# Performance work log

Measured on AMD Instinct MI355X. Metric: run time of the kernel, lower is better.

Reference implementation:

```python
import jax, jax.numpy as jnp
import numpy as np

B, T, D, VQ, L2, HID = 8, 2048, 768, 64, 12, 1024
K = 2 ** L2          # 4096 codebook entries
N_MID = 4            # condition_layer=6 -> 1 input + 4 middle + 1 output Linear, 5 BatchNorms
EPS_N = 1e-6
EPS_BN = 1e-5


def setup_inputs() -> dict:
    key = jax.random.key(0)
    ks = jax.random.split(key, 10)
    g = lambda i, shape, sc: jax.random.normal(ks[i], shape, jnp.float32) * sc
    return {
        "h_in": jax.random.normal(ks[0], (B, D, T), jnp.float32),
        "attn_mask": jax.random.randint(ks[1], (B, T), 0, 2, jnp.int32),
        "proj_w": g(2, (VQ, D), 0.02), "proj_b": jnp.zeros((VQ,), jnp.float32),
        "inv_w": g(3, (D, VQ), 0.02), "inv_b": jnp.zeros((D,), jnp.float32),
        "mlp_w_in": g(4, (HID, L2), 0.1), "mlp_b_in": jnp.zeros((HID,), jnp.float32),
        "mlp_w_mid": g(5, (N_MID, HID, HID), 0.03), "mlp_b_mid": jnp.zeros((N_MID, HID), jnp.float32),
        "mlp_w_out": g(6, (VQ, HID), 0.03), "mlp_b_out": jnp.zeros((VQ,), jnp.float32),
        "bn_gamma": jnp.ones((N_MID + 1, HID), jnp.float32),
        "bn_beta": jnp.zeros((N_MID + 1, HID), jnp.float32),
    }


def _bn(x, gamma, beta):
    # BatchNorm1d, training mode: batch mean / biased var over codebook rows
    m = x.mean(axis=0)
    v = x.var(axis=0)
    return (x - m) * jax.lax.rsqrt(v + EPS_BN) * gamma + beta


def _l2norm(x):
    return x / (jnp.linalg.norm(x, axis=-1, keepdims=True) + EPS_N)


def reference(h_in, attn_mask, proj_w, proj_b, inv_w, inv_b,
              mlp_w_in, mlp_b_in, mlp_w_mid, mlp_b_mid, mlp_w_out, mlp_b_out,
              bn_gamma, bn_beta):
    # --- codebook: binary vectors -> condition MLP (Linear+BN+ReLU x5, Linear) ---
    ints = jnp.arange(K)
    bits = ((ints[:, None] & (1 << jnp.arange(L2 - 1, -1, -1))) > 0).astype(jnp.float32)  # [K, L2]
    x = jax.nn.relu(_bn(bits @ mlp_w_in.T + mlp_b_in, bn_gamma[0], bn_beta[0]))
    for i in range(N_MID):
        x = jax.nn.relu(_bn(x @ mlp_w_mid[i].T + mlp_b_mid[i], bn_gamma[i + 1], bn_beta[i + 1]))
    embed = x @ mlp_w_out.T + mlp_b_out          # [K, VQ]
    embed = _l2norm(embed)                        # sphere=True

    # --- project hidden states: h_in [B,D,T] -> [B,T,VQ] ---
    h = jnp.einsum('bdt,vd->btv', h_in, proj_w) + proj_b
    h = _l2norm(h)

    # --- pairwise squared distances to codebook, argmax of -d (== softmax argmax) ---
    hf = h.reshape(-1, VQ)                                       # [B*T, VQ]
    d = (hf ** 2).sum(-1, keepdims=True) + (embed ** 2).sum(-1) - 2.0 * (hf @ embed.T)  # [B*T, K]
    code = jnp.argmax(-d, axis=-1)                               # [B*T]

    # --- masked gather/scatter quantization (eval path: hard codes) ---
    mask = (attn_mask == 1)                                      # [B, T]
    h_vq = embed[code].reshape(B, T, VQ) * mask[..., None].astype(h.dtype)
    quantized = jnp.einsum('btv,dv->btd', h_vq, inv_w) + inv_b   # proj_inv -> [B, T, D]
    vq_code = jnp.where(mask, code.reshape(B, T), 0)
    return quantized, vq_code
```

## Files before the change

kernel.cpp:

```cpp
#include <hip/hip_runtime.h>
#include <stddef.h>

#define BB   8
#define TT_  2048
#define DD   768
#define VQ_  64
#define L2C  12
#define HID_ 1024
#define KK   4096
#define NMID 4
#define NT   (BB*TT_)

typedef _Float16 h8v __attribute__((ext_vector_type(8)));
typedef float    f4v __attribute__((ext_vector_type(4)));

#define GL16(g, l) __builtin_amdgcn_global_load_lds( \
    (const __attribute__((address_space(1))) void*)(g), \
    (__attribute__((address_space(3))) void*)(l), 16, 0, 0)

__global__ __launch_bounds__(256) void k_mlp_in(const float* __restrict__ w_in,
                                                const float* __restrict__ b_in,
                                                float* __restrict__ X) {
    __shared__ float ws_[256 * 12];
    __shared__ float bs_[256];
    int tid = threadIdx.x;
    int h0  = blockIdx.x * 256;
    for (int i = tid; i < 256 * 12; i += 256) ws_[i] = w_in[h0 * 12 + i];
    bs_[tid] = b_in[h0 + tid];
    __syncthreads();
    float w[12];
#pragma unroll
    for (int l = 0; l < 12; l++) w[l] = ws_[tid * 12 + l];
    float bias = bs_[tid];
    int k0 = blockIdx.y * 16;
    for (int kk = 0; kk < 16; kk++) {
        int k = k0 + kk;
        float acc = bias;
#pragma unroll
        for (int l = 0; l < 12; l++)
            if ((k >> (11 - l)) & 1) acc += w[l];
        X[(size_t)k * HID_ + h0 + tid] = acc;
    }
}

__global__ __launch_bounds__(256) void k_bn_stats1(const float* __restrict__ Y,
                                                   float* __restrict__ part) {
    int b = blockIdx.x;
    int c = blockIdx.y * 256 + threadIdx.x;
    const float* src = Y + ((size_t)b << 6) * HID_ + c;
    float s = 0.f, q = 0.f;
    for (int r = 0; r < 64; r++) {
        float v = src[(size_t)r << 10];
        s += v; q += v * v;
    }
    part[((size_t)b << 10) + c] = s;
    part[65536 + ((size_t)b << 10) + c] = q;
}

__global__ __launch_bounds__(256) void k_bn_stats2(const float* __restrict__ part,
                                                   float* __restrict__ mv) {
    int c = blockIdx.x * 256 + threadIdx.x;
    float s = 0.f, q = 0.f;
    for (int b = 0; b < 64; b++) {
        s += part[((size_t)b << 10) + c];
        q += part[65536 + ((size_t)b << 10) + c];
    }
    float m = s * (1.f / KK);
    float v = q * (1.f / KK) - m * m;
    mv[c] = m; mv[HID_ + c] = v;
}

__global__ __launch_bounds__(256) void k_bn_apply_split(const float* __restrict__ Y,
                                                        const float* __restrict__ mv,
                                                        const float* __restrict__ gamma,
                                                        const float* __restrict__ beta,
                                                        _Float16* __restrict__ Xhi,
                                                        _Float16* __restrict__ Xlo) {
    int i = blockIdx.x * 256 + threadIdx.x;
    int c = (i << 2) & (HID_ - 1);
    float4 x = ((const float4*)Y)[i];
    float4 m = *(const float4*)(mv + c);
    float4 v = *(const float4*)(mv + HID_ + c);
    float4 g = *(const float4*)(gamma + c);
    float4 b = *(const float4*)(beta + c);
    float o[4];
    o[0] = fmaxf(0.f, (x.x - m.x) * (1.f / sqrtf(v.x + 1e-5f)) * g.x + b.x);
    o[1] = fmaxf(0.f, (x.y - m.y) * (1.f / sqrtf(v.y + 1e-5f)) * g.y + b.y);
    o[2] = fmaxf(0.f, (x.z - m.z) * (1.f / sqrtf(v.z + 1e-5f)) * g.z + b.z);
    o[3] = fmaxf(0.f, (x.w - m.w) * (1.f / sqrtf(v.w + 1e-5f)) * g.w + b.w);
    union { _Float16 h[4]; uint2 u; } uh, ul;
#pragma unroll
    for (int j = 0; j < 4; j++) {
        _Float16 h = (_Float16)o[j];
        uh.h[j] = h;
        ul.h[j] = (_Float16)(o[j] - (float)h);
    }
    *(uint2*)(Xhi + ((size_t)i << 2)) = uh.u;
    *(uint2*)(Xlo + ((size_t)i << 2)) = ul.u;
}

__global__ __launch_bounds__(256) void k_gemm_mfma2(const _Float16* __restrict__ Ahi,
                                                    const _Float16* __restrict__ Alo,
                                                    const _Float16* __restrict__ Whi,
                                                    const _Float16* __restrict__ Wlo,
                                                    const float* __restrict__ bias,
                                                    float* __restrict__ C,
                                                    int M, int N, int Kd) {
    __shared__ __attribute__((aligned(128))) char lds[2][24576];
    const int tid = threadIdx.x;
    int wg = blockIdx.x;
    const int nwg = gridDim.x;
    wg = (wg & 7) * (nwg >> 3) + (wg >> 3);
    const int nx = M >> 7;
    const int m0 = (wg % nx) << 7;
    const int n0 = (wg / nx) << 6;
    const int wave = tid >> 6, lane = tid & 63;
    const int l15 = lane & 15, quad = lane >> 4;
    const int wm = (wave >> 1) << 6;
    const int wn = (wave & 1) << 5;

    const int pA0 = ((wave << 1) | 0) * 1024 + lane * 16;
    const int pA1 = ((wave << 1) | 1) * 1024 + lane * 16;
    const int pW  = wave * 1024 + lane * 16;
    const int qA0 = pA0 ^ (((pA0 >> 7) & 3) << 4);
    const int qA1 = pA1 ^ (((pA1 >> 7) & 3) << 4);
    const int qW  = pW  ^ (((pW  >> 7) & 3) << 4);
    const size_t krow = (size_t)Kd * 2;
    const char* gAh0 = (const char*)Ahi + (size_t)(m0 + (qA0 >> 6)) * krow + (qA0 & 63);
    const char* gAh1 = (const char*)Ahi + (size_t)(m0 + (qA1 >> 6)) * krow + (qA1 & 63);
    const char* gAl0 = (const char*)Alo + (size_t)(m0 + (qA0 >> 6)) * krow + (qA0 & 63);
    const char* gAl1 = (const char*)Alo + (size_t)(m0 + (qA1 >> 6)) * krow + (qA1 & 63);
    const char* gWh  = (const char*)Whi + (size_t)(n0 + (qW >> 6)) * krow + (qW & 63);
    const char* gWl  = (const char*)Wlo + (size_t)(n0 + (qW >> 6)) * krow + (qW & 63);
    const int dA0 = (wave << 1) * 1024;
    const int dA1 = dA0 + 1024;
    const int dW  = wave * 1024;

    int offA[4], offW[2];
#pragma unroll
    for (int i = 0; i < 4; i++) {
        int r = wm + (i << 4) + l15;
        offA[i] = r * 64 + ((quad ^ ((r >> 1) & 3)) << 4);
    }
#pragma unroll
    for (int j = 0; j < 2; j++) {
        int r = wn + (j << 4) + l15;
        offW[j] = r * 64 + ((quad ^ ((r >> 1) & 3)) << 4);
    }

    f4v acc[4][2];
#pragma unroll
    for (int i = 0; i < 4; i++)
#pragma unroll
        for (int j = 0; j < 2; j++) acc[i][j] = (f4v){0.f, 0.f, 0.f, 0.f};

#define STAGE(bufi, tt) do { \
        char* b_ = lds[bufi]; size_t o_ = (size_t)(tt) << 6; \
        GL16(gAh0 + o_, b_ + dA0); \
        GL16(gAh1 + o_, b_ + dA1); \
        GL16(gAl0 + o_, b_ + 8192 + dA0); \
        GL16(gAl1 + o_, b_ + 8192 + dA1); \
        GL16(gWh  + o_, b_ + 16384 + dW); \
        GL16(gWl  + o_, b_ + 20480 + dW); \
    } while (0)

    STAGE(0, 0);
    const int nt = Kd >> 5;
    for (int t = 0; t < nt; ++t) {
        const int cur = t & 1;
        if (t + 1 < nt) {
            STAGE(cur ^ 1, t + 1);
            asm volatile("s_waitcnt vmcnt(6)" ::: "memory");
        } else {
            asm volatile("s_waitcnt vmcnt(0)" ::: "memory");
        }
        __builtin_amdgcn_s_barrier();
        asm volatile("" ::: "memory");
        const char* b = lds[cur];
        h8v ah[4], al[4], bh[2], bl[2];
#pragma unroll
        for (int i = 0; i < 4; i++) {
            ah[i] = *(const h8v*)(b + offA[i]);
            al[i] = *(const h8v*)(b + 8192 + offA[i]);
        }
#pragma unroll
        for (int j = 0; j < 2; j++) {
            bh[j] = *(const h8v*)(b + 16384 + offW[j]);
            bl[j] = *(const h8v*)(b + 20480 + offW[j]);
        }
        __builtin_amdgcn_s_setprio(1);
#pragma unroll
        for (int i = 0; i < 4; i++)
#pragma unroll
            for (int j = 0; j < 2; j++) {
                acc[i][j] = __builtin_amdgcn_mfma_f32_16x16x32_f16(ah[i], bh[j], acc[i][j], 0, 0, 0);
                acc[i][j] = __builtin_amdgcn_mfma_f32_16x16x32_f16(ah[i], bl[j], acc[i][j], 0, 0, 0);
                acc[i][j] = __builtin_amdgcn_mfma_f32_16x16x32_f16(al[i], bh[j], acc[i][j], 0, 0, 0);
            }
        __builtin_amdgcn_s_setprio(0);
        asm volatile("" ::: "memory");
        __builtin_amdgcn_s_barrier();
    }
#undef STAGE

#pragma unroll
    for (int j = 0; j < 2; j++) {
        int col = n0 + wn + (j << 4) + l15;
        float bv = bias[col];
#pragma unroll
        for (int i = 0; i < 4; i++) {
            int row = m0 + wm + (i << 4) + (quad << 2);
#pragma unroll
            for (int r = 0; r < 4; r++)
                C[(size_t)(row + r) * N + col] = acc[i][j][r] + bv;
        }
    }
}

__global__ __launch_bounds__(256) void k_l2norm(float* __restrict__ E,
                                                float* __restrict__ eqh,
                                                _Float16* __restrict__ Ehi,
                                                _Float16* __restrict__ Elo) {
    int tid = threadIdx.x;
    int row = blockIdx.x * 4 + (tid >> 6);
    int v = tid & 63;
    size_t off = ((size_t)row << 6) + v;
    float x = E[off];
    float ss = x * x;
#pragma unroll
    for (int o = 32; o; o >>= 1) ss += __shfl_xor(ss, o, 64);
    float inv = 1.f / (sqrtf(ss) + 1e-6f);
    float xn = x * inv;
    E[off] = xn;
    _Float16 hh = (_Float16)xn;
    Ehi[off] = hh;
    Elo[off] = (_Float16)(xn - (float)hh);
    if (v == 0) eqh[row] = -0.5f * (ss * inv * inv);
}

__global__ __launch_bounds__(256) void k_wsplit(const float* __restrict__ pw,
                                                _Float16* __restrict__ pwhi,
                                                _Float16* __restrict__ pwlo) {
    int i = blockIdx.x * 256 + threadIdx.x;
    float4 w = ((const float4*)pw)[i];
    float wf[4] = {w.x, w.y, w.z, w.w};
    union { _Float16 h[4]; uint2 u; } uh, ul;
#pragma unroll
    for (int j = 0; j < 4; j++) {
        _Float16 h = (_Float16)wf[j];
        uh.h[j] = h;
        ul.h[j] = (_Float16)(wf[j] - (float)h);
    }
    *(uint2*)(pwhi + ((size_t)i << 2)) = uh.u;
    *(uint2*)(pwlo + ((size_t)i << 2)) = ul.u;
}

__global__ __launch_bounds__(256) void k_cvt_inv(const float* __restrict__ iw,
                                                 _Float16* __restrict__ iwh) {
    int i = blockIdx.x * 256 + threadIdx.x;
    float4 w = ((const float4*)iw)[i];
    union { _Float16 h[4]; uint2 u; } uh;
    uh.h[0] = (_Float16)w.x; uh.h[1] = (_Float16)w.y;
    uh.h[2] = (_Float16)w.z; uh.h[3] = (_Float16)w.w;
    *(uint2*)(iwh + ((size_t)i << 2)) = uh.u;
}

__global__ __launch_bounds__(256) void k_proj_mfma(const float* __restrict__ h_in,
                                                   const _Float16* __restrict__ pwhi,
                                                   const _Float16* __restrict__ pwlo,
                                                   float* __restrict__ Hpart) {
    __shared__ float shA[128 * 33];
    const int tid = threadIdx.x;
    const int t0 = blockIdx.x * 128;
    const int ks = blockIdx.y;
    const int b = t0 >> 11;
    const int tloc0 = t0 & (TT_ - 1);
    const int wave = tid >> 6, lane = tid & 63;
    const int l15 = lane & 15, quad = lane >> 4;

    const int dl = tid >> 3;
    const int tg = (tid & 7) << 4;

    f4v acc[2][4];
#pragma unroll
    for (int i = 0; i < 2; i++)
#pragma unroll
        for (int j = 0; j < 4; j++) acc[i][j] = (f4v){0.f, 0.f, 0.f, 0.f};

    for (int kk = 0; kk < 6; kk++) {
        int dd0 = ks * 192 + kk * 32;
        const float* src = h_in + ((size_t)(b * DD + dd0 + dl) << 11) + tloc0 + tg;
        float4 g0 = *(const float4*)(src);
        float4 g1 = *(const float4*)(src + 4);
        float4 g2 = *(const float4*)(src + 8);
        float4 g3 = *(const float4*)(src + 12);
        __syncthreads();
        float gv[16] = {g0.x, g0.y, g0.z, g0.w, g1.x, g1.y, g1.z, g1.w,
                        g2.x, g2.y, g2.z, g2.w, g3.x, g3.y, g3.z, g3.w};
#pragma unroll
        for (int i = 0; i < 16; i++) shA[(tg + i) * 33 + dl] = gv[i];
        __syncthreads();

        h8v ah[2], al[2];
#pragma unroll
        for (int mt = 0; mt < 2; mt++) {
            const float* ap = &shA[((wave << 5) + (mt << 4) + l15) * 33 + (quad << 3)];
            float4 a0 = *(const float4*)(ap);
            float4 a1 = *(const float4*)(ap + 4);
            float av[8] = {a0.x, a0.y, a0.z, a0.w, a1.x, a1.y, a1.z, a1.w};
#pragma unroll
            for (int j = 0; j < 8; j++) {
                _Float16 h = (_Float16)av[j];
                ah[mt][j] = h;
                al[mt][j] = (_Float16)(av[j] - (float)h);
            }
        }
#pragma unroll
        for (int nt = 0; nt < 4; nt++) {
            size_t wb = (size_t)((nt << 4) + l15) * DD + dd0 + (quad << 3);
            h8v bh = *(const h8v*)(pwhi + wb);
            h8v bl = *(const h8v*)(pwlo + wb);
#pragma unroll
            for (int mt = 0; mt < 2; mt++) {
                acc[mt][nt] = __builtin_amdgcn_mfma_f32_16x16x32_f16(ah[mt], bh, acc[mt][nt], 0, 0, 0);
                acc[mt][nt] = __builtin_amdgcn_mfma_f32_16x16x32_f16(ah[mt], bl, acc[mt][nt], 0, 0, 0);
                acc[mt][nt] = __builtin_amdgcn_mfma_f32_16x16x32_f16(al[mt], bh, acc[mt][nt], 0, 0, 0);
            }
        }
    }
    float* dst = Hpart + ((size_t)ks << 20);
#pragma unroll
    for (int mt = 0; mt < 2; mt++) {
#pragma unroll
        for (int r = 0; r < 4; r++) {
            int t = t0 + (wave << 5) + (mt << 4) + (quad << 2) + r;
#pragma unroll
            for (int nt = 0; nt < 4; nt++)
                dst[((size_t)t << 6) + (nt << 4) + l15] = acc[mt][nt][r];
        }
    }
}

__global__ __launch_bounds__(256) void k_hnorm(const float* __restrict__ Hpart,
                                               const float* __restrict__ pb,
                                               _Float16* __restrict__ Hhi,
                                               _Float16* __restrict__ Hlo) {
    __shared__ float ssp[4][64];
    int tid = threadIdx.x;
    int tt = tid & 63, vg = tid >> 6;
    int t = blockIdx.x * 64 + tt;
    size_t base = ((size_t)t << 6) + (vg << 4);
    float o[16];
#pragma unroll
    for (int u = 0; u < 4; u++) {
        float4 p0 = *(const float4*)(Hpart + (0u << 20) + base + (u << 2));
        float4 p1 = *(const float4*)(Hpart + (1u << 20) + base + (u << 2));
        float4 p2 = *(const float4*)(Hpart + (2u << 20) + base + (u << 2));
        float4 p3 = *(const float4*)(Hpart + (3u << 20) + base + (u << 2));
        o[u * 4 + 0] = p0.x + p1.x + p2.x + p3.x;
        o[u * 4 + 1] = p0.y + p1.y + p2.y + p3.y;
        o[u * 4 + 2] = p0.z + p1.z + p2.z + p3.z;
        o[u * 4 + 3] = p0.w + p1.w + p2.w + p3.w;
    }
    float sp = 0.f;
#pragma unroll
    for (int j = 0; j < 16; j++) {
        o[j] += pb[(vg << 4) + j];
        sp = fmaf(o[j], o[j], sp);
    }
    ssp[vg][tt] = sp;
    __syncthreads();
    float ss = ssp[0][tt] + ssp[1][tt] + ssp[2][tt] + ssp[3][tt];
    float inv = 1.f / (sqrtf(ss) + 1e-6f);
    union { _Float16 h[8]; uint4 u; } uh0, uh1, ul0, ul1;
#pragma unroll
    for (int j = 0; j < 16; j++) {
        float xn = o[j] * inv;
        _Float16 hh = (_Float16)xn;
        _Float16 ll = (_Float16)(xn - (float)hh);
        if (j < 8) { uh0.h[j] = hh; ul0.h[j] = ll; }
        else       { uh1.h[j - 8] = hh; ul1.h[j - 8] = ll; }
    }
    *(uint4*)(Hhi + base)     = uh0.u;
    *(uint4*)(Hhi + base + 8) = uh1.u;
    *(uint4*)(Hlo + base)     = ul0.u;
    *(uint4*)(Hlo + base + 8) = ul1.u;
}

__global__ __launch_bounds__(256) void k_argmax_mfma(const _Float16* __restrict__ Hhi,
                                                     const _Float16* __restrict__ Hlo,
                                                     const _Float16* __restrict__ Ehi,
                                                     const _Float16* __restrict__ Elo,
                                                     const float* __restrict__ eqh,
                                                     float* __restrict__ ps,
                                                     int* __restrict__ pi) {
    int tid = threadIdx.x;
    int wave = tid >> 6, lane = tid & 63;
    int l15 = lane & 15, quad = lane >> 4;
    int t0 = blockIdx.x * 256 + wave * 64;
    int kh = blockIdx.y;
    const int kbase = kh << 8;

    h8v hh0[4], hh1[4], hl0[4], hl1[4];
#pragma unroll
    for (int s = 0; s < 4; s++) {
        size_t hb = (size_t)(t0 + (s << 4) + l15) * 64 + (quad << 3);
        hh0[s] = *(const h8v*)(Hhi + hb);
        hh1[s] = *(const h8v*)(Hhi + hb + 32);
        hl0[s] = *(const h8v*)(Hlo + hb);
        hl1[s] = *(const h8v*)(Hlo + hb + 32);
    }
    float best[4] = {-1e30f, -1e30f, -1e30f, -1e30f};
    int   idx[4]  = {0, 0, 0, 0};

    size_t eb = (size_t)(kbase + l15) * 64 + (quad << 3);
    h8v eh0 = *(const h8v*)(Ehi + eb);
    h8v eh1 = *(const h8v*)(Ehi + eb + 32);
    h8v el0 = *(const h8v*)(Elo + eb);
    h8v el1 = *(const h8v*)(Elo + eb + 32);
    float4 q4 = *(const float4*)(eqh + kbase + (quad << 2));

    for (int it = 0; it < 16; it++) {
        h8v ce0 = eh0, ce1 = eh1, cl0 = el0, cl1 = el1;
        float4 cq = q4;
        int k0 = kbase + (it << 4);
        int kn = k0 + 16;
        if (kn > KK - 16) kn = KK - 16;
        size_t ebn = (size_t)(kn + l15) * 64 + (quad << 3);
        eh0 = *(const h8v*)(Ehi + ebn);
        eh1 = *(const h8v*)(Ehi + ebn + 32);
        el0 = *(const h8v*)(Elo + ebn);
        el1 = *(const h8v*)(Elo + ebn + 32);
        q4 = *(const float4*)(eqh + kn + (quad << 2));

        f4v acc[4];
#pragma unroll
        for (int s = 0; s < 4; s++) acc[s] = (f4v){0.f, 0.f, 0.f, 0.f};
#pragma unroll
        for (int s = 0; s < 4; s++) acc[s] = __builtin_amdgcn_mfma_f32_16x16x32_f16(ce0, hh0[s], acc[s], 0, 0, 0);
#pragma unroll
        for (int s = 0; s < 4; s++) acc[s] = __builtin_amdgcn_mfma_f32_16x16x32_f16(ce1, hh1[s], acc[s], 0, 0, 0);
#pragma unroll
        for (int s = 0; s < 4; s++) acc[s] = __builtin_amdgcn_mfma_f32_16x16x32_f16(cl0, hh0[s], acc[s], 0, 0, 0);
#pragma unroll
        for (int s = 0; s < 4; s++) acc[s] = __builtin_amdgcn_mfma_f32_16x16x32_f16(cl1, hh1[s], acc[s], 0, 0, 0);
#pragma unroll
        for (int s = 0; s < 4; s++) acc[s] = __builtin_amdgcn_mfma_f32_16x16x32_f16(ce0, hl0[s], acc[s], 0, 0, 0);
#pragma unroll
        for (int s = 0; s < 4; s++) acc[s] = __builtin_amdgcn_mfma_f32_16x16x32_f16(ce1, hl1[s], acc[s], 0, 0, 0);
        float qv[4] = {cq.x, cq.y, cq.z, cq.w};
#pragma unroll
        for (int r = 0; r < 4; r++) {
            int k = k0 + (quad << 2) + r;
#pragma unroll
            for (int s = 0; s < 4; s++) {
                float sc = acc[s][r] + qv[r];
                if (sc > best[s]) { best[s] = sc; idx[s] = k; }
            }
        }
    }
#pragma unroll
    for (int m = 16; m <= 32; m <<= 1) {
#pragma unroll
        for (int s = 0; s < 4; s++) {
            float ob = __shfl_xor(best[s], m, 64);
            int   oi = __shfl_xor(idx[s], m, 64);
            if (ob > best[s] || (ob == best[s] && oi < idx[s])) { best[s] = ob; idx[s] = oi; }
        }
    }
    if (quad == 0) {
#pragma unroll
        for (int s = 0; s < 4; s++) {
            int t = t0 + (s << 4) + l15;
            ps[(size_t)t * 16 + kh] = best[s];
            pi[(size_t)t * 16 + kh] = idx[s];
        }
    }
}

__global__ __launch_bounds__(256) void k_merge(const float* __restrict__ ps,
                                               const int* __restrict__ pi,
                                               const int* __restrict__ mask,
                                               const _Float16* __restrict__ Ehi,
                                               _Float16* __restrict__ G16,
                                               float* __restrict__ outc) {
    __shared__ int codes[256];
    __shared__ int ms[256];
    int tid = threadIdx.x;
    int base = blockIdx.x << 8;
    int t = base + tid;
    float best = ps[(size_t)t * 16];
    int bi = pi[(size_t)t * 16];
#pragma unroll
    for (int s = 1; s < 16; s++) {
        float v = ps[(size_t)t * 16 + s];
        if (v > best) { best = v; bi = pi[(size_t)t * 16 + s]; }
    }
    int m = mask[t];
    codes[tid] = bi;
    ms[tid] = m;
    outc[t] = m ? (float)bi : 0.0f;
    __syncthreads();
    for (int i = tid; i < 256 * 8; i += 256) {
        int r = i >> 3, u = i & 7;
        uint4 e = ms[r] ? ((const uint4*)(Ehi + ((size_t)codes[r] << 6)))[u]
                        : make_uint4(0u, 0u, 0u, 0u);
        ((uint4*)(G16 + ((size_t)(base + r) << 6)))[u] = e;
    }
}

__global__ __launch_bounds__(256) void k_gemm_out(const _Float16* __restrict__ G16,
                                                  const _Float16* __restrict__ iwh,
                                                  const float* __restrict__ bias,
                                                  float* __restrict__ C) {
    const int tid = threadIdx.x;
    const int t0 = blockIdx.x * 128, n0 = blockIdx.y * 64;
    const int wave = tid >> 6, lane = tid & 63;
    const int l15 = lane & 15, quad = lane >> 4;

    f4v acc[2][4];
#pragma unroll
    for (int i = 0; i < 2; i++)
#pragma unroll
        for (int j = 0; j < 4; j++) acc[i][j] = (f4v){0.f, 0.f, 0.f, 0.f};

#pragma unroll
    for (int ks = 0; ks < 2; ks++) {
        int kk = (ks << 5) + (quad << 3);
        h8v a[2], b[4];
#pragma unroll
        for (int mt = 0; mt < 2; mt++)
            a[mt] = *(const h8v*)(G16 + (size_t)(t0 + (wave << 5) + (mt << 4) + l15) * 64 + kk);
#pragma unroll
        for (int nt = 0; nt < 4; nt++)
            b[nt] = *(const h8v*)(iwh + (size_t)(n0 + (nt << 4) + l15) * 64 + kk);
#pragma unroll
        for (int mt = 0; mt < 2; mt++)
#pragma unroll
            for (int nt = 0; nt < 4; nt++)
                acc[mt][nt] = __builtin_amdgcn_mfma_f32_16x16x32_f16(a[mt], b[nt], acc[mt][nt], 0, 0, 0);
    }
#pragma unroll
    for (int nt = 0; nt < 4; nt++) {
        int col = n0 + (nt << 4) + l15;
        float bv = bias[col];
#pragma unroll
        for (int mt = 0; mt < 2; mt++) {
            int row = t0 + (wave << 5) + (mt << 4) + (quad << 2);
#pragma unroll
            for (int r = 0; r < 4; r++)
                C[(size_t)(row + r) * DD + col] = acc[mt][nt][r] + bv;
        }
    }
}

extern "C" void kernel_launch(void* const* d_in, const int* in_sizes, int n_in,
                              void* d_out, int out_size, void* d_ws, size_t ws_size,
                              hipStream_t stream) {
    const float* h_in   = (const float*)d_in[0];
    const int*   amask  = (const int*)d_in[1];
    const float* proj_w = (const float*)d_in[2];
    const float* proj_b = (const float*)d_in[3];
    const float* inv_w  = (const float*)d_in[4];
    const float* inv_b  = (const float*)d_in[5];
    const float* w_in   = (const float*)d_in[6];
    const float* b_in   = (const float*)d_in[7];
    const float* w_mid  = (const float*)d_in[8];
    const float* b_mid  = (const float*)d_in[9];
    const float* w_out  = (const float*)d_in[10];
    const float* b_out  = (const float*)d_in[11];
    const float* gamma  = (const float*)d_in[12];
    const float* beta   = (const float*)d_in[13];

    float*     Y    = (float*)d_ws;
    _Float16*  Xhi  = (_Float16*)(Y + (size_t)KK * HID_);
    _Float16*  Xlo  = Xhi + (size_t)KK * HID_;
    float*     mv   = (float*)(Xlo + (size_t)KK * HID_);
    float*     Emb  = mv + 2 * HID_;
    float*     eqh  = Emb + (size_t)KK * VQ_;
    float*     spart= eqh + KK;
    _Float16*  pwhi = (_Float16*)(spart + 2 * 65536);
    _Float16*  pwlo = pwhi + (size_t)VQ_ * DD;
    float*    Hpart = Y;
    _Float16* H16hi = Xhi;
    _Float16* H16lo = H16hi + (size_t)NT * VQ_;
    _Float16* E16hi = H16lo + (size_t)NT * VQ_;
    _Float16* E16lo = E16hi + (size_t)KK * VQ_;
    float*    ps    = (float*)(E16lo + (size_t)KK * VQ_);
    int*      pidx  = (int*)(ps + (size_t)NT * 16);
    _Float16* G16   = (_Float16*)(pidx + (size_t)NT * 16);
    _Float16* iwh   = G16 + (size_t)NT * VQ_;

    float* out_q = (float*)d_out;
    float* out_c = out_q + (size_t)NT * DD;

    _Float16* Wmh = (_Float16*)d_out;
    _Float16* Wml = Wmh + (size_t)HID_ * HID_;
    _Float16* Woh = Wml + (size_t)HID_ * HID_;
    _Float16* Wol = Woh + (size_t)VQ_ * HID_;

    k_mlp_in<<<dim3(HID_ / 256, KK / 16), 256, 0, stream>>>(w_in, b_in, Y);
    k_bn_stats1<<<dim3(64, 4), 256, 0, stream>>>(Y, spart);
    k_bn_stats2<<<4, 256, 0, stream>>>(spart, mv);
    k_bn_apply_split<<<KK * HID_ / 1024, 256, 0, stream>>>(Y, mv, gamma, beta, Xhi, Xlo);
    for (int i = 0; i < NMID; i++) {
        k_wsplit<<<HID_ * HID_ / 1024, 256, 0, stream>>>(
            w_mid + (size_t)i * HID_ * HID_, Wmh, Wml);
        k_gemm_mfma2<<<(KK / 128) * (HID_ / 64), 256, 0, stream>>>(
            Xhi, Xlo, Wmh, Wml, b_mid + (size_t)i * HID_, Y, KK, HID_, HID_);
        k_bn_stats1<<<dim3(64, 4), 256, 0, stream>>>(Y, spart);
        k_bn_stats2<<<4, 256, 0, stream>>>(spart, mv);
        k_bn_apply_split<<<KK * HID_ / 1024, 256, 0, stream>>>(Y, mv,
            gamma + (size_t)(i + 1) * HID_, beta + (size_t)(i + 1) * HID_, Xhi, Xlo);
    }
    k_wsplit<<<VQ_ * HID_ / 1024, 256, 0, stream>>>(w_out, Woh, Wol);
    k_gemm_mfma2<<<(KK / 128) * (VQ_ / 64), 256, 0, stream>>>(
        Xhi, Xlo, Woh, Wol, b_out, Emb, KK, VQ_, HID_);
    k_l2norm<<<KK / 4, 256, 0, stream>>>(Emb, eqh, E16hi, E16lo);

    k_wsplit<<<VQ_ * DD / 1024, 256, 0, stream>>>(proj_w, pwhi, pwlo);
    k_cvt_inv<<<VQ_ * DD / 1024, 256, 0, stream>>>(inv_w, iwh);
    k_proj_mfma<<<dim3(NT / 128, 4), 256, 0, stream>>>(h_in, pwhi, pwlo, Hpart);
    k_hnorm<<<NT / 64, 256, 0, stream>>>(Hpart, proj_b, H16hi, H16lo);
    k_argmax_mfma<<<dim3(NT / 256, 16), 256, 0, stream>>>(
        H16hi, H16lo, E16hi, E16lo, eqh, ps, pidx);
    k_merge<<<NT / 256, 256, 0, stream>>>(ps, pidx, amask, E16hi, G16, out_c);
    k_gemm_out<<<dim3(NT / 128, DD / 64), 256, 0, stream>>>(G16, iwh, inv_b, out_q);
}
```

Measured before the change: 518.3 us.

## Use 128x128 tiled split-fp16 MFMA GEMM with 4-stage LDS pipeline for mid layers

Adds a specialized GEMM kernel for the 4096x1024x1024 middle MLP layers. It uses 128x128 output tiles instead of 128x64, and each wave computes a 64x64 block. Operands are staged through a 4-buffer LDS ring, loaded with direct global-to-LDS copies, with prefetch three steps ahead. The larger tile is meant to raise arithmetic intensity and cut redundant operand loads, and the deeper pipeline is meant to hide memory latency. The cost is fewer workgroups (256), 128KB of LDS per block which limits occupancy to one block per CU, and a higher accumulator register count.

```diff
diff --git a/kernel.cpp b/kernel.cpp
--- a/kernel.cpp
+++ b/kernel.cpp
@@ -99,6 +99,100 @@
     *(uint2*)(Xlo + ((size_t)i << 2)) = ul.u;
 }
 
+__global__ __launch_bounds__(256) void k_gemm_mfma3(const _Float16* __restrict__ Ahi,
+                                                    const _Float16* __restrict__ Alo,
+                                                    const _Float16* __restrict__ Whi,
+                                                    const _Float16* __restrict__ Wlo,
+                                                    const float* __restrict__ bias,
+                                                    float* __restrict__ C) {
+    __shared__ __attribute__((aligned(128))) char lds[4 * 32768];
+    const int tid = threadIdx.x;
+    const int wg = blockIdx.x;
+    const int m0 = (wg & 31) << 7;
+    const int n0 = (wg >> 5) << 7;
+    const int wave = tid >> 6, lane = tid & 63;
+    const int l15 = lane & 15, quad = lane >> 4;
+    const int wm = (wave >> 1) << 6;
+    const int wn = (wave & 1) << 6;
+
+    const int rowA = (wave << 5) + (lane >> 2);
+    const int colb = (lane & 3) << 4;
+    const char* gA_h = (const char*)Ahi + ((size_t)(m0 + rowA) << 11) + colb;
+    const char* gA_l = (const char*)Alo + ((size_t)(m0 + rowA) << 11) + colb;
+    const char* gW_h = (const char*)Whi + ((size_t)(n0 + rowA) << 11) + colb;
+    const char* gW_l = (const char*)Wlo + ((size_t)(n0 + rowA) << 11) + colb;
+    const int dA = wave << 11;
+
+    int offA[4], offW[4];
+#pragma unroll
+    for (int i = 0; i < 4; i++) offA[i] = ((wm + (i << 4) + l15) << 6) + (quad << 4);
+#pragma unroll
+    for (int j = 0; j < 4; j++) offW[j] = ((wn + (j << 4) + l15) << 6) + (quad << 4);
+
+    f4v acc[4][4];
+#pragma unroll
+    for (int i = 0; i < 4; i++)
+#pragma unroll
+        for (int j = 0; j < 4; j++) acc[i][j] = (f4v){0.f, 0.f, 0.f, 0.f};
+
+#define STG(bufi, tt) do { \
+        char* b_ = lds + ((bufi) << 15); int o_ = (tt) << 6; \
+        GL16(gA_h + o_,         b_ + dA); \
+        GL16(gA_h + 32768 + o_, b_ + dA + 1024); \
+        GL16(gA_l + o_,         b_ + 8192 + dA); \
+        GL16(gA_l + 32768 + o_, b_ + 8192 + dA + 1024); \
+        GL16(gW_h + o_,         b_ + 16384 + dA); \
+        GL16(gW_h + 32768 + o_, b_ + 16384 + dA + 1024); \
+        GL16(gW_l + o_,         b_ + 24576 + dA); \
+        GL16(gW_l + 32768 + o_, b_ + 24576 + dA + 1024); \
+    } while (0)
+
+    STG(0, 0); STG(1, 1); STG(2, 2);
+    for (int t = 0; t < 32; ++t) {
+        if (t <= 29)      asm volatile("s_waitcnt vmcnt(16)" ::: "memory");
+        else if (t == 30) asm volatile("s_waitcnt vmcnt(8)"  ::: "memory");
+        else              asm volatile("s_waitcnt vmcnt(0)"  ::: "memory");
+        __builtin_amdgcn_s_barrier();
+        asm volatile("" ::: "memory");
+        if (t + 3 < 32) STG((t + 3) & 3, t + 3);
+        const char* b = lds + ((size_t)(t & 3) << 15);
+        h8v ah[4], al[4];
+#pragma unroll
+        for (int i = 0; i < 4; i++) {
+            ah[i] = *(const h8v*)(b + offA[i]);
+            al[i] = *(const h8v*)(b + 8192 + offA[i]);
+        }
+        __builtin_amdgcn_s_setprio(1);
+#pragma unroll
+        for (int j = 0; j < 4; j++) {
+            h8v bh = *(const h8v*)(b + 16384 + offW[j]);
+            h8v bl = *(const h8v*)(b + 24576 + offW[j]);
+#pragma unroll
+            for (int i = 0; i < 4; i++) {
+                acc[i][j] = __builtin_amdgcn_mfma_f32_16x16x32_f16(ah[i], bh, acc[i][j], 0, 0, 0);
+                acc[i][j] = __builtin_amdgcn_mfma_f32_16x16x32_f16(ah[i], bl, acc[i][j], 0, 0, 0);
+                acc[i][j] = __builtin_amdgcn_mfma_f32_16x16x32_f16(al[i], bh, acc[i][j], 0, 0, 0);
+            }
+        }
+        __builtin_amdgcn_s_setprio(0);
+        asm volatile("" ::: "memory");
+    }
+#undef STG
+
+#pragma unroll
+    for (int j = 0; j < 4; j++) {
+        int col = n0 + wn + (j << 4) + l15;
+        float bv = bias[col];
+#pragma unroll
+        for (int i = 0; i < 4; i++) {
+            int row = m0 + wm + (i << 4) + (quad << 2);
+#pragma unroll
+            for (int r = 0; r < 4; r++)
+                C[(size_t)(row + r) * HID_ + col] = acc[i][j][r] + bv;
+        }
+    }
+}
+
 __global__ __launch_bounds__(256) void k_gemm_mfma2(const _Float16* __restrict__ Ahi,
                                                     const _Float16* __restrict__ Alo,
                                                     const _Float16* __restrict__ Whi,
@@ -606,8 +700,8 @@
     for (int i = 0; i < NMID; i++) {
         k_wsplit<<<HID_ * HID_ / 1024, 256, 0, stream>>>(
             w_mid + (size_t)i * HID_ * HID_, Wmh, Wml);
-        k_gemm_mfma2<<<(KK / 128) * (HID_ / 64), 256, 0, stream>>>(
-            Xhi, Xlo, Wmh, Wml, b_mid + (size_t)i * HID_, Y, KK, HID_, HID_);
+        k_gemm_mfma3<<<(KK / 128) * (HID_ / 128), 256, 0, stream>>>(
+            Xhi, Xlo, Wmh, Wml, b_mid + (size_t)i * HID_, Y);
         k_bn_stats1<<<dim3(64, 4), 256, 0, stream>>>(Y, spart);
         k_bn_stats2<<<4, 256, 0, stream>>>(spart, mv);
         k_bn_apply_split<<<KK * HID_ / 1024, 256, 0, stream>>>(Y, mv,
```

Result: faster. 473.5 us (-8.7%).
